# Kernel optimization log

Measured on AMD Instinct MI355X. Metric: run time of the kernel, lower is better.

## Reference

```python
import jax, jax.numpy as jnp
import numpy as np

S = 7
B = 2
C = 20
LAMBDA_NOOBJ = 0.5
EPS = 1e-9  # guards IoU division; original divides by raw union


def setup_inputs() -> dict:
    key = jax.random.key(0)
    k1, k2 = jax.random.split(key)
    N = 8192
    preds = jax.random.uniform(k1, (N, S, S, B * (5 + C)), dtype=jnp.float32)
    targets = jax.random.uniform(k2, (N, S, S, B * (5 + C)), dtype=jnp.float32)
    return {"preds": preds, "targets": targets}


def _iou_xywh(a, b):
    # a, b: (..., 4) in (cx, cy, w, h); returns (...,) IoU
    ax1 = a[..., 0] - a[..., 2] / 2
    ay1 = a[..., 1] - a[..., 3] / 2
    ax2 = a[..., 0] + a[..., 2] / 2
    ay2 = a[..., 1] + a[..., 3] / 2
    bx1 = b[..., 0] - b[..., 2] / 2
    by1 = b[..., 1] - b[..., 3] / 2
    bx2 = b[..., 0] + b[..., 2] / 2
    by2 = b[..., 1] + b[..., 3] / 2
    iw = jnp.clip(jnp.minimum(ax2, bx2) - jnp.maximum(ax1, bx1), 0.0)
    ih = jnp.clip(jnp.minimum(ay2, by2) - jnp.maximum(ay1, by1), 0.0)
    inter = iw * ih
    union = a[..., 2] * a[..., 3] + b[..., 2] * b[..., 3] - inter
    return inter / (union + EPS)


def reference(preds, targets):
    N = preds.shape[0]
    p = preds.reshape(N, S, S, B, 5 + C)
    t = targets.reshape(N, S, S, B, 5 + C)

    # per-cell, per-slot IoU between pred box b and target box b: (N,S,S,B)
    ious = _iou_xywh(p[..., :4], t[..., :4])

    # best-box selection per cell
    best = jnp.argmax(ious, axis=-1)                       # (N,S,S)
    best_oh = jax.nn.one_hot(best, B, dtype=preds.dtype)   # (N,S,S,B)

    # object presence from target confidence of any box slot
    has_object = jnp.any(t[..., 4] > 0.0, axis=-1)         # (N,S,S)

    # 1) position loss (x,y) for the responsible box in object cells
    dxy = jnp.sum((p[..., 0:2] - t[..., 0:2]) ** 2, axis=-1)     # (N,S,S,B)
    pos_loss = jnp.sum(best_oh * dxy, axis=-1)                   # (N,S,S)
    loss = jnp.sum(jnp.where(has_object, pos_loss, 0.0))

    # 2) class loss (last C entries of the cell vector) for every cell
    pc = p[..., -1, 5:]   # (N,S,S,C)
    tc = t[..., -1, 5:]
    loss = loss + jnp.sum((pc - tc) ** 2)

    # 3) confidence loss: pred_conf = iou_b * p_class[gt], target_conf = iou_b
    gt_cls = jnp.argmax(tc, axis=-1)                                    # (N,S,S)
    p_gt = jnp.take_along_axis(pc, gt_cls[..., None], axis=-1)[..., 0]  # (N,S,S)
    conf_err = (ious * p_gt[..., None] - ious) ** 2                     # (N,S,S,B)
    w = jnp.where(best_oh > 0, 1.0, LAMBDA_NOOBJ)
    loss = loss + jnp.sum(w * conf_err)

    return loss / N
```

## Files before the change

kernel.cpp:

```cpp
#include <hip/hip_runtime.h>


#define NPC 50
#define CPB 128
#define TPB 128

typedef const __attribute__((address_space(1))) void gvoid_t;
typedef __attribute__((address_space(3))) void lvoid_t;

__device__ __forceinline__ float iou_xywh(float px, float py, float pw, float ph,
                                          float tx, float ty, float tw, float th) {
    float ax1 = px - pw * 0.5f, ay1 = py - ph * 0.5f;
    float ax2 = px + pw * 0.5f, ay2 = py + ph * 0.5f;
    float bx1 = tx - tw * 0.5f, by1 = ty - th * 0.5f;
    float bx2 = tx + tw * 0.5f, by2 = ty + th * 0.5f;
    float iw = fmaxf(fminf(ax2, bx2) - fmaxf(ax1, bx1), 0.0f);
    float ih = fmaxf(fminf(ay2, by2) - fmaxf(ay1, by1), 0.0f);
    float inter = iw * ih;
    float uni = pw * ph + tw * th - inter;
    return inter / (uni + 1e-9f);
}

__global__ __launch_bounds__(TPB) void yolo_partial_kernel(
        const float* __restrict__ preds,
        const float* __restrict__ targets,
        float* __restrict__ part,
        int ncells) {
    __shared__ float lp[CPB * NPC];
    __shared__ float lt[CPB * NPC];
    __shared__ float wsum[TPB / 64];

    const int tid = threadIdx.x;
    const int wave = tid >> 6;
    const int lane = tid & 63;
    const long long cell0 = (long long)blockIdx.x * CPB;
    const long long base = cell0 * NPC;
    const int cells_here = min(CPB, ncells - (int)cell0);

    if (cells_here == CPB) {
        const float* src = (wave == 0) ? (preds + base) : (targets + base);
        float* dst = (wave == 0) ? lp : lt;
        #pragma unroll
        for (int c = 0; c < 25; ++c) {
            __builtin_amdgcn_global_load_lds(
                (gvoid_t*)(src + c * 256 + lane * 4),
                (lvoid_t*)(dst + c * 256),
                16, 0, 0);
        }
        asm volatile("s_waitcnt vmcnt(0)" ::: "memory");
    } else {
        const int f_total = cells_here * NPC;
        for (int i = tid; i < f_total; i += TPB) {
            lp[i] = preds[base + i];
            lt[i] = targets[base + i];
        }
    }
    __syncthreads();

    float cell = 0.0f;
    if ((int)cell0 + tid < ncells) {
        const float2* cp2 = (const float2*)(lp + tid * NPC);
        const float2* ct2 = (const float2*)(lt + tid * NPC);

        float2 p01 = cp2[0];
        float2 p23 = cp2[1];
        float2 t01 = ct2[0];
        float2 t23 = ct2[1];
        float2 t4_ = ct2[2];
        float2 pA = cp2[12];
        float2 pB = cp2[13];
        float2 pC = cp2[14];
        float2 tA = ct2[12];
        float2 tB = ct2[13];
        float2 tC = ct2[14];

        float iou0 = iou_xywh(p01.x, p01.y, p23.x, p23.y,
                              t01.x, t01.y, t23.x, t23.y);
        float iou1 = iou_xywh(pA.y, pB.x, pB.y, pC.x,
                              tA.y, tB.x, tB.y, tC.x);
        int best = (iou1 > iou0) ? 1 : 0;
        bool has_obj = (t4_.x > 0.0f) || (tC.y > 0.0f);

        float dx, dy;
        if (best == 0) { dx = p01.x - t01.x; dy = p01.y - t01.y; }
        else           { dx = pA.y - tA.y;   dy = pB.x - tB.x;   }
        float dxy = dx * dx + dy * dy;
        cell = has_obj ? dxy : 0.0f;

        float csum = 0.0f;
        float bv = -1e30f;
        float pg = 0.0f;
        #pragma unroll
        for (int j = 0; j < 10; ++j) {
            float2 tv = ct2[15 + j];
            float2 pv = cp2[15 + j];
            float d0 = pv.x - tv.x;
            float d1 = pv.y - tv.y;
            csum += d0 * d0 + d1 * d1;
            if (tv.x > bv) { bv = tv.x; pg = pv.x; }
            if (tv.y > bv) { bv = tv.y; pg = pv.y; }
        }
        cell += csum;

        float f = pg - 1.0f;
        float f2 = f * f;
        float e0 = iou0 * iou0 * f2;
        float e1 = iou1 * iou1 * f2;
        cell += (best == 0) ? e0 : 0.5f * e0;
        cell += (best == 1) ? e1 : 0.5f * e1;
    }

    float v = cell;
    #pragma unroll
    for (int off = 32; off >= 1; off >>= 1) v += __shfl_down(v, off);
    if (lane == 0) wsum[wave] = v;
    __syncthreads();
    if (tid == 0) {
        float s = 0.0f;
        #pragma unroll
        for (int w = 0; w < TPB / 64; ++w) s += wsum[w];
        part[blockIdx.x] = s;
    }
}

__global__ __launch_bounds__(256) void yolo_final_kernel(
        const float* __restrict__ part, float* __restrict__ out,
        int nblk, float invN) {
    __shared__ float wsum[4];
    const int tid = threadIdx.x;
    float s = 0.0f;
    for (int i = tid; i < nblk; i += 256) s += part[i];
    #pragma unroll
    for (int off = 32; off >= 1; off >>= 1) s += __shfl_down(s, off);
    if ((tid & 63) == 0) wsum[tid >> 6] = s;
    __syncthreads();
    if (tid == 0) {
        out[0] = (wsum[0] + wsum[1] + wsum[2] + wsum[3]) * invN;
    }
}

extern "C" void kernel_launch(void* const* d_in, const int* in_sizes, int n_in,
                              void* d_out, int out_size, void* d_ws, size_t ws_size,
                              hipStream_t stream) {
    const float* preds = (const float*)d_in[0];
    const float* targets = (const float*)d_in[1];
    float* out = (float*)d_out;
    float* part = (float*)d_ws;

    const int ncells = in_sizes[0] / NPC;
    const int N = ncells / 49;
    const int nblk = (ncells + CPB - 1) / CPB;

    yolo_partial_kernel<<<nblk, TPB, 0, stream>>>(preds, targets, part, ncells);
    yolo_final_kernel<<<1, 256, 0, stream>>>(part, out, nblk, 1.0f / (float)N);
}
```

Measured before the change: 33.78 us.

## Replace LDS staging with direct per-thread global loads of cell data

Drops the coalesced global-to-LDS bulk copy and has each thread read its own 50-float cell straight from global memory as float2 loads. Block size goes from 128 to 256 threads, which halves the number of partial sums. This removes the LDS traffic, the vmcnt wait and the barrier before compute. The cost is uncoalesced strided access: each lane reads from addresses 200 bytes apart, so caches have to absorb the scattered loads and effective bandwidth may drop.

```diff
diff --git a/kernel.cpp b/kernel.cpp
--- a/kernel.cpp
+++ b/kernel.cpp
@@ -2,11 +2,7 @@
 
 
 #define NPC 50
-#define CPB 128
-#define TPB 128
-
-typedef const __attribute__((address_space(1))) void gvoid_t;
-typedef __attribute__((address_space(3))) void lvoid_t;
+#define TPB 256
 
 __device__ __forceinline__ float iou_xywh(float px, float py, float pw, float ph,
                                           float tx, float ty, float tw, float th) {
@@ -21,46 +17,20 @@
     return inter / (uni + 1e-9f);
 }
 
-__global__ __launch_bounds__(TPB) void yolo_partial_kernel(
+__global__ __launch_bounds__(TPB) void yolo_cell_kernel(
         const float* __restrict__ preds,
         const float* __restrict__ targets,
         float* __restrict__ part,
         int ncells) {
-    __shared__ float lp[CPB * NPC];
-    __shared__ float lt[CPB * NPC];
     __shared__ float wsum[TPB / 64];
 
     const int tid = threadIdx.x;
-    const int wave = tid >> 6;
-    const int lane = tid & 63;
-    const long long cell0 = (long long)blockIdx.x * CPB;
-    const long long base = cell0 * NPC;
-    const int cells_here = min(CPB, ncells - (int)cell0);
-
-    if (cells_here == CPB) {
-        const float* src = (wave == 0) ? (preds + base) : (targets + base);
-        float* dst = (wave == 0) ? lp : lt;
-        #pragma unroll
-        for (int c = 0; c < 25; ++c) {
-            __builtin_amdgcn_global_load_lds(
-                (gvoid_t*)(src + c * 256 + lane * 4),
-                (lvoid_t*)(dst + c * 256),
-                16, 0, 0);
-        }
-        asm volatile("s_waitcnt vmcnt(0)" ::: "memory");
-    } else {
-        const int f_total = cells_here * NPC;
-        for (int i = tid; i < f_total; i += TPB) {
-            lp[i] = preds[base + i];
-            lt[i] = targets[base + i];
-        }
-    }
-    __syncthreads();
+    const int cell_idx = blockIdx.x * TPB + tid;
 
     float cell = 0.0f;
-    if ((int)cell0 + tid < ncells) {
-        const float2* cp2 = (const float2*)(lp + tid * NPC);
-        const float2* ct2 = (const float2*)(lt + tid * NPC);
+    if (cell_idx < ncells) {
+        const float2* cp2 = (const float2*)(preds + (long long)cell_idx * NPC);
+        const float2* ct2 = (const float2*)(targets + (long long)cell_idx * NPC);
 
         float2 p01 = cp2[0];
         float2 p23 = cp2[1];
@@ -113,6 +83,8 @@
     float v = cell;
     #pragma unroll
     for (int off = 32; off >= 1; off >>= 1) v += __shfl_down(v, off);
+    const int wave = tid >> 6;
+    const int lane = tid & 63;
     if (lane == 0) wsum[wave] = v;
     __syncthreads();
     if (tid == 0) {
@@ -149,8 +121,8 @@
 
     const int ncells = in_sizes[0] / NPC;
     const int N = ncells / 49;
-    const int nblk = (ncells + CPB - 1) / CPB;
+    const int nblk = (ncells + TPB - 1) / TPB;
 
-    yolo_partial_kernel<<<nblk, TPB, 0, stream>>>(preds, targets, part, ncells);
+    yolo_cell_kernel<<<nblk, TPB, 0, stream>>>(preds, targets, part, ncells);
     yolo_final_kernel<<<1, 256, 0, stream>>>(part, out, nblk, 1.0f / (float)N);
 }
```

Result: slower. 45.40 us (+34.4%).
